# Kernel optimization log

Measured on AMD Instinct MI355X. Metric: run time of the kernel, lower is better.

Reference implementation:

```python
import jax, jax.numpy as jnp
import numpy as np

N_NODES = 100000
N_EDGES = 1600000
NUM_FEAT = 64
DIM = 32
K = 3  # num_stacks
T = 2  # num_layers


def setup_inputs() -> dict:
    key = jax.random.key(0)
    ks = jax.random.split(key, 10)
    g = lambda k, s, fan: jax.random.normal(k, s, jnp.float32) * (1.0 / np.sqrt(fan))
    x = jax.random.normal(ks[0], (N_NODES, NUM_FEAT), jnp.float32)
    edge_index = jax.random.randint(ks[1], (2, N_EDGES), 0, N_NODES)
    return {
        "x": x,
        "edge_index": edge_index,
        "w1_init": g(ks[2], (K, NUM_FEAT, DIM), NUM_FEAT),
        "w1": g(ks[3], (1, K, DIM, DIM), DIM),
        "w1_root": g(ks[4], (1, K, NUM_FEAT, DIM), NUM_FEAT),
        "b1": jnp.zeros((1, K, 1, DIM), jnp.float32),
        "w2_init": g(ks[5], (K, DIM, DIM), DIM),
        "w2": g(ks[6], (1, K, DIM, DIM), DIM),
        "w2_root": g(ks[7], (1, K, DIM, DIM), DIM),
        "b2": jnp.zeros((1, K, 1, DIM), jnp.float32),
    }


def _gcn_norm(src, dst, num_nodes):
    # symmetric normalization WITHOUT self loops (PyG ARMAConv default)
    deg = jax.ops.segment_sum(jnp.ones(src.shape[0], jnp.float32), dst, num_segments=num_nodes)
    dinv = jnp.where(deg > 0, jax.lax.rsqrt(jnp.maximum(deg, 1.0)), 0.0)
    return dinv[src] * dinv[dst]  # [E]


def _arma_conv(x, src, dst, norm, init_w, w, root_w, b, act):
    # x: [N,F_in]; init_w: [K,F_in,F_out]; w/root_w/b: shared (leading dim 1)
    num_nodes = x.shape[0]
    out = jnp.einsum('nf,kfo->kno', x, init_w)          # [K,N,F_out]
    root_term = jnp.einsum('nf,kfo->kno', x, root_w[0])  # shared across layers
    bias = b[0]                                          # [K,1,F_out]

    def prop(o):  # o: [N,F_out] -> A_hat @ o
        return jax.ops.segment_sum(o[src] * norm[:, None], dst, num_segments=num_nodes)

    for t in range(T):
        if t > 0:
            out = jnp.einsum('knf,kfo->kno', out, w[0])
        out = jax.vmap(prop)(out)
        out = act(out + root_term + bias)
    return out.mean(axis=0)  # mean over stacks -> [N,F_out]


def reference(x, edge_index, w1_init, w1, w1_root, b1, w2_init, w2, w2_root, b2):
    src, dst = edge_index[0], edge_index[1]
    norm = _gcn_norm(src, dst, x.shape[0])
    # eval mode: dropout is identity
    h = jax.nn.relu(_arma_conv(x, src, dst, norm, w1_init, w1, w1_root, b1, jax.nn.relu))
    out = _arma_conv(h, src, dst, norm, w2_init, w2, w2_root, b2, lambda z: z)
    return out
```

## Files before the change

### kernel.cpp

```cpp
#include <hip/hip_runtime.h>
#include <hip/hip_bf16.h>


#define KSTACK 3
#define DIM    32
#define FDIM   96
#define NB     256
#define TILE   4096

typedef __hip_bfloat16 bf16;
typedef _Float16 f16;
typedef _Float16 halfx2 __attribute__((ext_vector_type(2)));

__device__ __forceinline__ float dot2h(unsigned int a, unsigned int b, float c) {
#if __has_builtin(__builtin_amdgcn_fdot2)
    return __builtin_amdgcn_fdot2(__builtin_bit_cast(halfx2, a),
                                  __builtin_bit_cast(halfx2, b), c, false);
#else
    halfx2 ha = __builtin_bit_cast(halfx2, a);
    halfx2 hb = __builtin_bit_cast(halfx2, b);
    return c + (float)ha.x * (float)hb.x + (float)ha.y * (float)hb.y;
#endif
}

__device__ __forceinline__ unsigned int pkh(float lo, float hi) {
    return __builtin_bit_cast(unsigned int, __builtin_amdgcn_cvt_pkrtz(lo, hi));
}

__device__ __forceinline__ halfx2 h2(unsigned int q) {
    return __builtin_bit_cast(halfx2, q);
}


__global__ void zero_int_kernel(int* __restrict__ p, int n) {
    int i = blockIdx.x * 256 + threadIdx.x;
    if (i < n) p[i] = 0;
}

__global__ __launch_bounds__(256) void bucket_hist_kernel(const int* __restrict__ dst,
                                                          int* __restrict__ bcnt, int E) {
    __shared__ int cnt[NB];
    for (int i = threadIdx.x; i < NB; i += 256) cnt[i] = 0;
    __syncthreads();
    const int e0 = blockIdx.x * TILE;
    const int count = min(TILE, E - e0);
    for (int u = threadIdx.x; u < count; u += 256)
        atomicAdd(&cnt[dst[e0 + u] >> 9], 1);
    __syncthreads();
    for (int i = threadIdx.x; i < NB; i += 256)
        if (cnt[i]) atomicAdd(&bcnt[i], cnt[i]);
}

__global__ __launch_bounds__(256) void bucket_scan_kernel(const int* __restrict__ bcnt,
                                                          int* __restrict__ gcur,
                                                          int* __restrict__ gbase) {
    __shared__ int s[NB];
    const int t = threadIdx.x;
    int v = bcnt[t];
    s[t] = v;
    __syncthreads();
    for (int off = 1; off < NB; off <<= 1) {
        int add = (t >= off) ? s[t - off] : 0;
        __syncthreads();
        s[t] += add;
        __syncthreads();
    }
    gcur[t]  = s[t] - v;
    gbase[t] = s[t] - v;
}

__global__ __launch_bounds__(256) void group_edges_kernel(
    const int* __restrict__ src, const int* __restrict__ dst,
    int* __restrict__ gcur, int2* __restrict__ grouped, int E)
{
    __shared__ int cnt[NB], pref[NB], lbase[NB], lofs[NB], gres[NB];
    __shared__ int2 stage[TILE];
    const int tid = threadIdx.x;
    const int e0 = blockIdx.x * TILE;
    const int count = min(TILE, E - e0);
    cnt[tid] = 0;
    __syncthreads();
    #pragma unroll
    for (int u = 0; u < TILE / 256; ++u) {
        int idx = u * 256 + tid;
        if (idx < count) atomicAdd(&cnt[dst[e0 + idx] >> 9], 1);
    }
    __syncthreads();
    int v = cnt[tid];
    pref[tid] = v;
    __syncthreads();
    for (int off = 1; off < NB; off <<= 1) {
        int add = (tid >= off) ? pref[tid - off] : 0;
        __syncthreads();
        pref[tid] += add;
        __syncthreads();
    }
    int ex = pref[tid] - v;
    lbase[tid] = ex;
    lofs[tid]  = ex;
    gres[tid] = atomicAdd(&gcur[tid], v);
    __syncthreads();
    #pragma unroll
    for (int u = 0; u < TILE / 256; ++u) {
        int idx = u * 256 + tid;
        if (idx < count) {
            int e = e0 + idx;
            int d = dst[e];
            int lp = atomicAdd(&lofs[d >> 9], 1);
            stage[lp] = make_int2(src[e] << 6, d);
        }
    }
    __syncthreads();
    for (int i = tid; i < count; i += 256) {
        int2 pr = stage[i];
        int b = pr.y >> 9;
        grouped[gres[b] + (i - lbase[b])] = pr;
    }
}

__global__ __launch_bounds__(256) void deg_from_grouped_kernel(
    const int2* __restrict__ grouped, const int* __restrict__ gbase,
    const int* __restrict__ bcnt, int* __restrict__ deg, int N)
{
    __shared__ int h[512];
    const int b  = blockIdx.x;
    const int nb = b * 512;
    for (int i = threadIdx.x; i < 512; i += 256) h[i] = 0;
    __syncthreads();
    const int e0 = gbase[b], cnt = bcnt[b];
    for (int u = threadIdx.x; u < cnt; u += 256)
        atomicAdd(&h[grouped[e0 + u].y & 511], 1);
    __syncthreads();
    for (int i = threadIdx.x; i < 512; i += 256)
        if (nb + i < N) deg[nb + i] = h[i];
}

__global__ void dinv_kernel(const int* __restrict__ deg, float* __restrict__ dinv, int N) {
    int i = blockIdx.x * 256 + threadIdx.x;
    if (i < N) {
        int d = deg[i];
        dinv[i] = (d > 0) ? rsqrtf((float)d) : 0.0f;
    }
}

__global__ __launch_bounds__(512) void scan1_kernel(const int* __restrict__ deg,
                                                    int* __restrict__ off4,
                                                    int* __restrict__ bsums, int N) {
    __shared__ int tmp[512];
    int t = threadIdx.x;
    int i = blockIdx.x * 512 + t;
    int v = (i < N) ? ((deg[i] + 3) & ~3) : 0;
    tmp[t] = v;
    __syncthreads();
    for (int off = 1; off < 512; off <<= 1) {
        int add = (t >= off) ? tmp[t - off] : 0;
        __syncthreads();
        tmp[t] += add;
        __syncthreads();
    }
    if (i <= N) off4[i] = tmp[t] - v;
    if (t == 511) bsums[blockIdx.x] = tmp[511];
}

__global__ void scan2_kernel(int* __restrict__ bsums, int nb) {
    if (blockIdx.x == 0 && threadIdx.x == 0) {
        int run = 0;
        for (int b = 0; b < nb; ++b) { int v = bsums[b]; bsums[b] = run; run += v; }
    }
}

__global__ void scan3_kernel(int* __restrict__ off4, const int* __restrict__ bsums, int N) {
    int i = blockIdx.x * 256 + threadIdx.x;
    if (i <= N) off4[i] += bsums[i >> 9];
}

__global__ __launch_bounds__(256) void fill_csr_bucket_kernel(
    const int2* __restrict__ grouped, const int* __restrict__ gbase,
    const int* __restrict__ bcnt, const int* __restrict__ off4,
    int* __restrict__ csr, int N, int dummy)
{
    __shared__ int lofs[512];
    const int b  = blockIdx.x;
    const int nb = b * 512;
    for (int i = threadIdx.x; i < 512; i += 256)
        lofs[i] = (nb + i < N) ? off4[nb + i] : 0;
    __syncthreads();
    const int e0 = gbase[b], cnt = bcnt[b];
    for (int u = threadIdx.x; u < cnt; u += 256) {
        int2 pr = grouped[e0 + u];
        int pos = atomicAdd(&lofs[pr.y & 511], 1);
        csr[pos] = pr.x;
    }
    __syncthreads();
    for (int i = threadIdx.x; i < 512; i += 256) {
        int n = nb + i;
        if (n < N) {
            int p = lofs[i];
            int e = off4[n + 1];
            for (; p < e; ++p) csr[p] = dummy;
        }
    }
}

__global__ void zero_dummy_kernel(f16* __restrict__ a, f16* __restrict__ b,
                                  f16* __restrict__ c, int N) {
    int t = threadIdx.x;
    if (t < FDIM) {
        a[(long)N * FDIM + t] = (f16)0.f;
        b[(long)N * FDIM + t] = (f16)0.f;
    }
    if (t < DIM) c[(long)N * DIM + t] = (f16)0.f;
}


template <int FIN, bool MEANROOT, bool XF16>
__global__ __launch_bounds__(256) void mm_init_kernel(
    const float* __restrict__ xf,
    const f16*   __restrict__ xh,
    const float* __restrict__ wA,
    const float* __restrict__ wB,
    const float* __restrict__ dinv,
    f16*   __restrict__ outA,
    f16*   __restrict__ rootb,
    float* __restrict__ rootm,
    const float* __restrict__ bias,
    int N)
{
    constexpr int F2 = FIN / 2;
    __shared__ unsigned int swA2[KSTACK * F2 * 32];
    __shared__ unsigned int swB2[KSTACK * F2 * 32];
    __shared__ unsigned int sx2[F2 * 64];
    const int tid = threadIdx.x;
    const int n0  = blockIdx.x * 64;

    for (int i = tid; i < KSTACK * F2 * 32; i += 256) {
        int k = i / (F2 * 32), r = i % (F2 * 32), f2 = r >> 5, o = r & 31;
        swA2[i] = pkh(wA[(k * FIN + 2 * f2) * 32 + o], wA[(k * FIN + 2 * f2 + 1) * 32 + o]);
        swB2[i] = pkh(wB[(k * FIN + 2 * f2) * 32 + o], wB[(k * FIN + 2 * f2 + 1) * 32 + o]);
    }
    for (int i = tid; i < 64 * F2; i += 256) {
        int jj = i / F2, f2 = i % F2;
        int n = n0 + jj; if (n >= N) n = N - 1;
        unsigned int v;
        if (XF16) v = *reinterpret_cast<const unsigned int*>(xh + (long)n * FIN + 2 * f2);
        else      v = pkh(xf[(long)n * FIN + 2 * f2], xf[(long)n * FIN + 2 * f2 + 1]);
        sx2[f2 * 64 + jj] = v;
    }
    __syncthreads();

    const int o = tid & 31;
    const int g = tid >> 5;
    float bz[KSTACK];
    #pragma unroll
    for (int k = 0; k < KSTACK; ++k) bz[k] = bias[k * 32 + o];
    float accA[8][KSTACK];
    float accB[8][KSTACK];
    #pragma unroll
    for (int jj = 0; jj < 8; ++jj)
        #pragma unroll
        for (int k = 0; k < KSTACK; ++k) { accA[jj][k] = 0.f; accB[jj][k] = 0.f; }

    #pragma unroll 2
    for (int f2 = 0; f2 < F2; ++f2) {
        uint4 xlo = *reinterpret_cast<const uint4*>(&sx2[f2 * 64 + 8 * g]);
        uint4 xhi = *reinterpret_cast<const uint4*>(&sx2[f2 * 64 + 8 * g + 4]);
        unsigned int xp[8] = {xlo.x, xlo.y, xlo.z, xlo.w, xhi.x, xhi.y, xhi.z, xhi.w};
        #pragma unroll
        for (int k = 0; k < KSTACK; ++k) {
            unsigned int wa2 = swA2[(k * F2 + f2) * 32 + o];
            unsigned int wb2 = swB2[(k * F2 + f2) * 32 + o];
            #pragma unroll
            for (int jj = 0; jj < 8; ++jj) {
                accA[jj][k] = dot2h(xp[jj], wa2, accA[jj][k]);
                accB[jj][k] = dot2h(xp[jj], wb2, accB[jj][k]);
            }
        }
    }

    #pragma unroll
    for (int jj = 0; jj < 8; ++jj) {
        long n = n0 + 8 * g + jj;
        if (n < N) {
            const float di = dinv[n];
            float rsum = 0.f;
            #pragma unroll
            for (int k = 0; k < KSTACK; ++k) {
                float rb = accB[jj][k] + bz[k];
                outA[n * FDIM + k * 32 + o]  = (f16)(accA[jj][k] * di);
                rootb[n * FDIM + k * 32 + o] = (f16)rb;
                rsum += rb;
            }
            if (MEANROOT)
                rootm[n * 32 + o] = rsum * (1.0f / 3.0f);
        }
    }
}


#define GATHER_LOOP8()                                                         \
    const int m = max(nA, nB);                                                 \
    halfx2 aA01a = {0, 0}, aA23a = {0, 0}, aA01b = {0, 0}, aA23b = {0, 0};     \
    halfx2 aB01a = {0, 0}, aB23a = {0, 0}, aB01b = {0, 0}, aB23b = {0, 0};     \
    for (int b = 0; b < m; b += 8) {                                           \
        int4 tA0 = *reinterpret_cast<const int4*>(csr + iA + b);               \
        int4 tA1 = *reinterpret_cast<const int4*>(csr + iA + b + 4);           \
        int4 tB0 = *reinterpret_cast<const int4*>(csr + iB + b);               \
        int4 tB1 = *reinterpret_cast<const int4*>(csr + iB + b + 4);           \
        const int rA = nA - b, rB = nB - b;                                    \
        int oA0 = rA > 0 ? tA0.x : dummy;                                      \
        int oA1 = rA > 1 ? tA0.y : dummy;                                      \
        int oA2 = rA > 2 ? tA0.z : dummy;                                      \
        int oA3 = rA > 3 ? tA0.w : dummy;                                      \
        int oA4 = rA > 4 ? tA1.x : dummy;                                      \
        int oA5 = rA > 5 ? tA1.y : dummy;                                      \
        int oA6 = rA > 6 ? tA1.z : dummy;                                      \
        int oA7 = rA > 7 ? tA1.w : dummy;                                      \
        int oB0 = rB > 0 ? tB0.x : dummy;                                      \
        int oB1 = rB > 1 ? tB0.y : dummy;                                      \
        int oB2 = rB > 2 ? tB0.z : dummy;                                      \
        int oB3 = rB > 3 ? tB0.w : dummy;                                      \
        int oB4 = rB > 4 ? tB1.x : dummy;                                      \
        int oB5 = rB > 5 ? tB1.y : dummy;                                      \
        int oB6 = rB > 6 ? tB1.z : dummy;                                      \
        int oB7 = rB > 7 ? tB1.w : dummy;                                      \
        if (ld) {                                                              \
            uint2 qA0 = *reinterpret_cast<const uint2*>(base + 3 * oA0 + lb);  \
            uint2 qA1 = *reinterpret_cast<const uint2*>(base + 3 * oA1 + lb);  \
            uint2 qA2 = *reinterpret_cast<const uint2*>(base + 3 * oA2 + lb);  \
            uint2 qA3 = *reinterpret_cast<const uint2*>(base + 3 * oA3 + lb);  \
            uint2 qA4 = *reinterpret_cast<const uint2*>(base + 3 * oA4 + lb);  \
            uint2 qA5 = *reinterpret_cast<const uint2*>(base + 3 * oA5 + lb);  \
            uint2 qA6 = *reinterpret_cast<const uint2*>(base + 3 * oA6 + lb);  \
            uint2 qA7 = *reinterpret_cast<const uint2*>(base + 3 * oA7 + lb);  \
            uint2 qB0 = *reinterpret_cast<const uint2*>(base + 3 * oB0 + lb);  \
            uint2 qB1 = *reinterpret_cast<const uint2*>(base + 3 * oB1 + lb);  \
            uint2 qB2 = *reinterpret_cast<const uint2*>(base + 3 * oB2 + lb);  \
            uint2 qB3 = *reinterpret_cast<const uint2*>(base + 3 * oB3 + lb);  \
            uint2 qB4 = *reinterpret_cast<const uint2*>(base + 3 * oB4 + lb);  \
            uint2 qB5 = *reinterpret_cast<const uint2*>(base + 3 * oB5 + lb);  \
            uint2 qB6 = *reinterpret_cast<const uint2*>(base + 3 * oB6 + lb);  \
            uint2 qB7 = *reinterpret_cast<const uint2*>(base + 3 * oB7 + lb);  \
            aA01a += h2(qA0.x); aA23a += h2(qA0.y);                            \
            aA01b += h2(qA1.x); aA23b += h2(qA1.y);                            \
            aA01a += h2(qA2.x); aA23a += h2(qA2.y);                            \
            aA01b += h2(qA3.x); aA23b += h2(qA3.y);                            \
            aA01a += h2(qA4.x); aA23a += h2(qA4.y);                            \
            aA01b += h2(qA5.x); aA23b += h2(qA5.y);                            \
            aA01a += h2(qA6.x); aA23a += h2(qA6.y);                            \
            aA01b += h2(qA7.x); aA23b += h2(qA7.y);                            \
            aB01a += h2(qB0.x); aB23a += h2(qB0.y);                            \
            aB01b += h2(qB1.x); aB23b += h2(qB1.y);                            \
            aB01a += h2(qB2.x); aB23a += h2(qB2.y);                            \
            aB01b += h2(qB3.x); aB23b += h2(qB3.y);                            \
            aB01a += h2(qB4.x); aB23a += h2(qB4.y);                            \
            aB01b += h2(qB5.x); aB23b += h2(qB5.y);                            \
            aB01a += h2(qB6.x); aB23a += h2(qB6.y);                            \
            aB01b += h2(qB7.x); aB23b += h2(qB7.y);                            \
        }                                                                      \
    }                                                                          \
    const float aA0 = (float)aA01a.x + (float)aA01b.x;                         \
    const float aA1 = (float)aA01a.y + (float)aA01b.y;                         \
    const float aA2 = (float)aA23a.x + (float)aA23b.x;                         \
    const float aA3 = (float)aA23a.y + (float)aA23b.y;                         \
    const float aB0 = (float)aB01a.x + (float)aB01b.x;                         \
    const float aB1 = (float)aB01a.y + (float)aB01b.y;                         \
    const float aB2 = (float)aB23a.x + (float)aB23b.x;                         \
    const float aB3 = (float)aB23a.y + (float)aB23b.y;

#define DST_SETUP()                                                            \
    const int dA = blockIdx.x * 16 + j;                                        \
    const int dB = dA + 8;                                                     \
    const bool vA = dA < N, vB = dB < N;                                       \
    const int dummy = N * 64;                                                  \
    const bool ld  = lane < 24;                                                \
    const int  lb  = lane * 8;                                                 \
    const char* base = (const char*)in;                                        \
    halfx2 rA01 = {0, 0}, rA23 = {0, 0}, rB01 = {0, 0}, rB23 = {0, 0};         \
    int iA = 0, nA = 0, iB = 0, nB = 0;                                        \
    float diA = 0.f, diB = 0.f;                                                \
    if (vA) {                                                                  \
        iA = off4[dA]; nA = off4[dA + 1] - iA; diA = dinv[dA];                 \
        if (ld) {                                                              \
            uint2 rr = *reinterpret_cast<const uint2*>(                        \
                (const char*)root + (long)dA * 192 + lb);                      \
            rA01 = h2(rr.x); rA23 = h2(rr.y);                                  \
        }                                                                      \
    }                                                                          \
    if (vB) {                                                                  \
        iB = off4[dB]; nB = off4[dB + 1] - iB; diB = dinv[dB];                 \
        if (ld) {                                                              \
            uint2 rr = *reinterpret_cast<const uint2*>(                        \
                (const char*)root + (long)dB * 192 + lb);                      \
            rB01 = h2(rr.x); rB23 = h2(rr.y);                                  \
        }                                                                      \
    }

__device__ __forceinline__ void gemv96(const unsigned int* __restrict__ sv,
                                       const unsigned int* __restrict__ sw2,
                                       int lane, float& r0, float& r1, float& r2) {
    float o[KSTACK];
    #pragma unroll
    for (int k = 0; k < KSTACK; ++k) {
        const unsigned int* sp = sv + k * 16;
        uint4 s0 = *reinterpret_cast<const uint4*>(sp);
        uint4 s1 = *reinterpret_cast<const uint4*>(sp + 4);
        uint4 s2 = *reinterpret_cast<const uint4*>(sp + 8);
        uint4 s3 = *reinterpret_cast<const uint4*>(sp + 12);
        const unsigned int* wp = sw2 + k * 512 + lane;
        float a = 0.f;
        a = dot2h(s0.x, wp[0],   a); a = dot2h(s0.y, wp[32],  a);
        a = dot2h(s0.z, wp[64],  a); a = dot2h(s0.w, wp[96],  a);
        a = dot2h(s1.x, wp[128], a); a = dot2h(s1.y, wp[160], a);
        a = dot2h(s1.z, wp[192], a); a = dot2h(s1.w, wp[224], a);
        a = dot2h(s2.x, wp[256], a); a = dot2h(s2.y, wp[288], a);
        a = dot2h(s2.z, wp[320], a); a = dot2h(s2.w, wp[352], a);
        a = dot2h(s3.x, wp[384], a); a = dot2h(s3.y, wp[416], a);
        a = dot2h(s3.z, wp[448], a); a = dot2h(s3.w, wp[480], a);
        o[k] = a;
    }
    r0 = o[0]; r1 = o[1]; r2 = o[2];
}

__global__ __launch_bounds__(256) void prop_mm_kernel(
    const f16*   __restrict__ in,
    const int*   __restrict__ off4,
    const int*   __restrict__ csr,
    const float* __restrict__ dinv,
    const f16*   __restrict__ root,
    const float* __restrict__ w,
    f16* __restrict__ out, int N)
{
    __shared__ unsigned int sw2[KSTACK * 512];
    __shared__ unsigned int sv2[16][48];
    const int tid = threadIdx.x;
    for (int i = tid; i < KSTACK * 512; i += 256) {
        int k = i >> 9, r = i & 511, t = r >> 5, o = r & 31;
        sw2[i] = pkh(w[(k * 32 + 2 * t) * 32 + o], w[(k * 32 + 2 * t + 1) * 32 + o]);
    }
    __syncthreads();
    const int lane = tid & 31;
    const int j    = tid >> 5;
    DST_SETUP();

    GATHER_LOOP8();

    if (ld) {
        if (vA) {
            float v0 = fmaxf(aA0 * diA + (float)rA01.x, 0.f);
            float v1 = fmaxf(aA1 * diA + (float)rA01.y, 0.f);
            float v2 = fmaxf(aA2 * diA + (float)rA23.x, 0.f);
            float v3 = fmaxf(aA3 * diA + (float)rA23.y, 0.f);
            sv2[j][2 * lane]     = pkh(v0, v1);
            sv2[j][2 * lane + 1] = pkh(v2, v3);
        }
        if (vB) {
            float v0 = fmaxf(aB0 * diB + (float)rB01.x, 0.f);
            float v1 = fmaxf(aB1 * diB + (float)rB01.y, 0.f);
            float v2 = fmaxf(aB2 * diB + (float)rB23.x, 0.f);
            float v3 = fmaxf(aB3 * diB + (float)rB23.y, 0.f);
            sv2[j + 8][2 * lane]     = pkh(v0, v1);
            sv2[j + 8][2 * lane + 1] = pkh(v2, v3);
        }
    }
    if (vA) {
        float o0, o1, o2;
        gemv96(&sv2[j][0], sw2, lane, o0, o1, o2);
        out[(long)dA * FDIM + lane]      = (f16)(o0 * diA);
        out[(long)dA * FDIM + 32 + lane] = (f16)(o1 * diA);
        out[(long)dA * FDIM + 64 + lane] = (f16)(o2 * diA);
    }
    if (vB) {
        float o0, o1, o2;
        gemv96(&sv2[j + 8][0], sw2, lane, o0, o1, o2);
        out[(long)dB * FDIM + lane]      = (f16)(o0 * diB);
        out[(long)dB * FDIM + 32 + lane] = (f16)(o1 * diB);
        out[(long)dB * FDIM + 64 + lane] = (f16)(o2 * diB);
    }
}

__global__ __launch_bounds__(256) void prop_mean_kernel(
    const f16*   __restrict__ in,
    const int*   __restrict__ off4,
    const int*   __restrict__ csr,
    const float* __restrict__ dinv,
    const f16*   __restrict__ root,
    f16* __restrict__ out,
    int N)
{
    __shared__ float sv[16][FDIM];
    const int tid = threadIdx.x;
    const int lane = tid & 31;
    const int j    = tid >> 5;
    DST_SETUP();

    GATHER_LOOP8();

    if (ld) {
        if (vA) {
            sv[j][4*lane]   = fmaxf(aA0 * diA + (float)rA01.x, 0.f);
            sv[j][4*lane+1] = fmaxf(aA1 * diA + (float)rA01.y, 0.f);
            sv[j][4*lane+2] = fmaxf(aA2 * diA + (float)rA23.x, 0.f);
            sv[j][4*lane+3] = fmaxf(aA3 * diA + (float)rA23.y, 0.f);
        }
        if (vB) {
            sv[j+8][4*lane]   = fmaxf(aB0 * diB + (float)rB01.x, 0.f);
            sv[j+8][4*lane+1] = fmaxf(aB1 * diB + (float)rB01.y, 0.f);
            sv[j+8][4*lane+2] = fmaxf(aB2 * diB + (float)rB23.x, 0.f);
            sv[j+8][4*lane+3] = fmaxf(aB3 * diB + (float)rB23.y, 0.f);
        }
    }
    if (vA) {
        float mv = fmaxf((sv[j][lane] + sv[j][32 + lane] + sv[j][64 + lane]) * (1.0f / 3.0f), 0.f);
        out[(long)dA * 32 + lane] = (f16)mv;
    }
    if (vB) {
        float mv = fmaxf((sv[j+8][lane] + sv[j+8][32 + lane] + sv[j+8][64 + lane]) * (1.0f / 3.0f), 0.f);
        out[(long)dB * 32 + lane] = (f16)mv;
    }
}

__global__ __launch_bounds__(256) void prop_mm_mean_kernel(
    const f16*   __restrict__ in,
    const int*   __restrict__ off4,
    const int*   __restrict__ csr,
    const float* __restrict__ dinv,
    const f16*   __restrict__ root,
    const float* __restrict__ w,
    f16* __restrict__ out, int N)
{
    __shared__ unsigned int sw2[KSTACK * 512];
    __shared__ unsigned int sv2[16][48];
    const int tid = threadIdx.x;
    for (int i = tid; i < KSTACK * 512; i += 256) {
        int k = i >> 9, r = i & 511, t = r >> 5, o = r & 31;
        sw2[i] = pkh(w[(k * 32 + 2 * t) * 32 + o], w[(k * 32 + 2 * t + 1) * 32 + o]);
    }
    __syncthreads();
    const int lane = tid & 31;
    const int j    = tid >> 5;
    DST_SETUP();

    GATHER_LOOP8();

    if (ld) {
        if (vA) {
            sv2[j][2 * lane]     = pkh(aA0 * diA + (float)rA01.x, aA1 * diA + (float)rA01.y);
            sv2[j][2 * lane + 1] = pkh(aA2 * diA + (float)rA23.x, aA3 * diA + (float)rA23.y);
        }
        if (vB) {
            sv2[j + 8][2 * lane]     = pkh(aB0 * diB + (float)rB01.x, aB1 * diB + (float)rB01.y);
            sv2[j + 8][2 * lane + 1] = pkh(aB2 * diB + (float)rB23.x, aB3 * diB + (float)rB23.y);
        }
    }
    if (vA) {
        float o0, o1, o2;
        gemv96(&sv2[j][0], sw2, lane, o0, o1, o2);
        out[(long)dA * 32 + lane] = (f16)((o0 + o1 + o2) * (diA * (1.0f / 3.0f)));
    }
    if (vB) {
        float o0, o1, o2;
        gemv96(&sv2[j + 8][0], sw2, lane, o0, o1, o2);
        out[(long)dB * 32 + lane] = (f16)((o0 + o1 + o2) * (diB * (1.0f / 3.0f)));
    }
}

__global__ __launch_bounds__(256) void prop_mean2_kernel(
    const f16*   __restrict__ in,
    const int*   __restrict__ off4,
    const int*   __restrict__ csr,
    const float* __restrict__ dinv,
    const float* __restrict__ rootm,
    float* __restrict__ out,
    int N)
{
    const int lane = threadIdx.x & 15;
    const int g    = threadIdx.x >> 4;
    const int d    = blockIdx.x * 16 + g;
    if (d >= N) return;
    const int dummy = N * 64;
    const int lb = lane * 4;
    const char* base = (const char*)in;
    const int i0 = off4[d];
    const int n  = off4[d + 1] - i0;
    halfx2 aa = {0, 0}, ab = {0, 0};
    for (int b = 0; b < n; b += 8) {
        int4 t0 = *reinterpret_cast<const int4*>(csr + i0 + b);
        int4 t1 = *reinterpret_cast<const int4*>(csr + i0 + b + 4);
        const int r = n - b;
        int o0 = r > 0 ? t0.x : dummy;
        int o1 = r > 1 ? t0.y : dummy;
        int o2 = r > 2 ? t0.z : dummy;
        int o3 = r > 3 ? t0.w : dummy;
        int o4 = r > 4 ? t1.x : dummy;
        int o5 = r > 5 ? t1.y : dummy;
        int o6 = r > 6 ? t1.z : dummy;
        int o7 = r > 7 ? t1.w : dummy;
        unsigned int q0 = *reinterpret_cast<const unsigned int*>(base + o0 + lb);
        unsigned int q1 = *reinterpret_cast<const unsigned int*>(base + o1 + lb);
        unsigned int q2 = *reinterpret_cast<const unsigned int*>(base + o2 + lb);
        unsigned int q3 = *reinterpret_cast<const unsigned int*>(base + o3 + lb);
        unsigned int q4 = *reinterpret_cast<const unsigned int*>(base + o4 + lb);
        unsigned int q5 = *reinterpret_cast<const unsigned int*>(base + o5 + lb);
        unsigned int q6 = *reinterpret_cast<const unsigned int*>(base + o6 + lb);
        unsigned int q7 = *reinterpret_cast<const unsigned int*>(base + o7 + lb);
        aa += h2(q0); ab += h2(q1); aa += h2(q2); ab += h2(q3);
        aa += h2(q4); ab += h2(q5); aa += h2(q6); ab += h2(q7);
    }
    const float di = dinv[d];
    float a0 = (float)aa.x + (float)ab.x;
    float a1 = (float)aa.y + (float)ab.y;
    float2 rm = *reinterpret_cast<const float2*>(rootm + (long)d * 32 + 2 * lane);
    float2 res = make_float2(a0 * di + rm.x, a1 * di + rm.y);
    *reinterpret_cast<float2*>(out + (long)d * 32 + 2 * lane) = res;
}


extern "C" void kernel_launch(void* const* d_in, const int* in_sizes, int n_in,
                              void* d_out, int out_size, void* d_ws, size_t ws_size,
                              hipStream_t stream) {
    const float* x       = (const float*)d_in[0];
    const int*   edge    = (const int*)  d_in[1];
    const float* w1_init = (const float*)d_in[2];
    const float* w1      = (const float*)d_in[3];
    const float* w1_root = (const float*)d_in[4];
    const float* b1      = (const float*)d_in[5];
    const float* w2_init = (const float*)d_in[6];
    const float* w2      = (const float*)d_in[7];
    const float* w2_root = (const float*)d_in[8];
    const float* b2      = (const float*)d_in[9];
    float* out = (float*)d_out;

    const int N = in_sizes[0] / 64;
    const int E = in_sizes[1] / 2;
    const int* src = edge;
    const int* dst = edge + E;
    const int E4max = E + 3 * N;

    char* p = (char*)d_ws;
    auto alloc = [&](size_t bytes) { void* r = (void*)p; p += (bytes + 255) & ~(size_t)255; return r; };
    int*   deg      = (int*)  alloc((size_t)N * 4);
    float* dinv     = (float*)alloc((size_t)N * 4);
    int*   off4     = (int*)  alloc((size_t)(N + 1) * 4);
    const int nScanBlocks = (N + 1 + 511) / 512;
    int*   bsums    = (int*)  alloc((size_t)nScanBlocks * 4);
    int*   bcnt     = (int*)  alloc((size_t)NB * 4);
    int*   gcur     = (int*)  alloc((size_t)NB * 4);
    int*   gbase    = (int*)  alloc((size_t)NB * 4);
    int*   csr_boff = (int*)  alloc((size_t)(E4max + 1024) * 4);
    f16*   gatherA  = (f16*)  alloc((size_t)(N + 1) * FDIM * 2);
    f16*   gatherB  = (f16*)  alloc((size_t)(N + 1) * FDIM * 2);
    f16*   grow2    = (f16*)  alloc((size_t)(N + 1) * DIM * 2);
    f16*   rootb    = (f16*)  alloc((size_t)N * FDIM * 2);
    float* rootm    = (float*)alloc((size_t)N * DIM * 4);
    f16*   hbuf     = (f16*)  alloc((size_t)N * DIM * 2);
    int2*  grouped  = (int2*) alloc((size_t)E * 8);
    (void)ws_size; (void)n_in; (void)out_size;

    const int gN     = (N + 255) / 256;
    const int gN1    = (N + 1 + 255) / 256;
    const int gT     = (E + TILE - 1) / TILE;
    const int gNod64 = (N + 63) / 64;
    const int gNod16 = (N + 15) / 16;

    zero_int_kernel<<<1, 256, 0, stream>>>(bcnt, NB);
    bucket_hist_kernel<<<gT, 256, 0, stream>>>(dst, bcnt, E);
    bucket_scan_kernel<<<1, NB, 0, stream>>>(bcnt, gcur, gbase);
    group_edges_kernel<<<gT, 256, 0, stream>>>(src, dst, gcur, grouped, E);
    deg_from_grouped_kernel<<<NB, 256, 0, stream>>>(grouped, gbase, bcnt, deg, N);
    dinv_kernel<<<gN, 256, 0, stream>>>(deg, dinv, N);
    scan1_kernel<<<nScanBlocks, 512, 0, stream>>>(deg, off4, bsums, N);
    scan2_kernel<<<1, 64, 0, stream>>>(bsums, nScanBlocks);
    scan3_kernel<<<gN1, 256, 0, stream>>>(off4, bsums, N);
    fill_csr_bucket_kernel<<<NB, 256, 0, stream>>>(grouped, gbase, bcnt, off4, csr_boff, N, N * 64);
    zero_dummy_kernel<<<1, 96, 0, stream>>>(gatherA, gatherB, grow2, N);

    mm_init_kernel<64, false, false><<<gNod64, 256, 0, stream>>>(x, nullptr, w1_init, w1_root, dinv, gatherA, rootb, nullptr, b1, N);
    prop_mm_kernel<<<gNod16, 256, 0, stream>>>(gatherA, off4, csr_boff, dinv, rootb, w1, gatherB, N);
    prop_mean_kernel<<<gNod16, 256, 0, stream>>>(gatherB, off4, csr_boff, dinv, rootb, hbuf, N);

    mm_init_kernel<32, true, true><<<gNod64, 256, 0, stream>>>(nullptr, hbuf, w2_init, w2_root, dinv, gatherA, rootb, rootm, b2, N);
    prop_mm_mean_kernel<<<gNod16, 256, 0, stream>>>(gatherA, off4, csr_boff, dinv, rootb, w2, grow2, N);
    prop_mean2_kernel<<<gNod16, 256, 0, stream>>>(grow2, off4, csr_boff, dinv, rootm, out, N);
}
```

Measured before the change: 361.1 us.

## Pack grouped edges into 32-bit words and fuse degree, dinv, and scan

Grouped edge records shrink from int2 to a single 32-bit word holding the local destination index in the high 9 bits and the source in the low 23 bits. The per-bucket degree histogram, the dinv computation and the first scan stage are merged into one kernel, which removes two launches and the deg buffer round trip. The serial single-thread block-sum scan becomes a parallel 256-thread scan. This relies on N fitting in 23 bits and on the scan block count matching the bucket count, and it caps scan2 at 256 blocks.

```diff
diff --git a/kernel.cpp b/kernel.cpp
--- a/kernel.cpp
+++ b/kernel.cpp
@@ -71,7 +71,7 @@
 
 __global__ __launch_bounds__(256) void group_edges_kernel(
     const int* __restrict__ src, const int* __restrict__ dst,
-    int* __restrict__ gcur, int2* __restrict__ grouped, int E)
+    int* __restrict__ gcur, unsigned int* __restrict__ grouped, int E)
 {
     __shared__ int cnt[NB], pref[NB], lbase[NB], lofs[NB], gres[NB];
     __shared__ int2 stage[TILE];
@@ -107,49 +107,38 @@
             int e = e0 + idx;
             int d = dst[e];
             int lp = atomicAdd(&lofs[d >> 9], 1);
-            stage[lp] = make_int2(src[e] << 6, d);
+            stage[lp] = make_int2(src[e], d);
         }
     }
     __syncthreads();
     for (int i = tid; i < count; i += 256) {
         int2 pr = stage[i];
         int b = pr.y >> 9;
-        grouped[gres[b] + (i - lbase[b])] = pr;
-    }
-}
-
-__global__ __launch_bounds__(256) void deg_from_grouped_kernel(
-    const int2* __restrict__ grouped, const int* __restrict__ gbase,
-    const int* __restrict__ bcnt, int* __restrict__ deg, int N)
+        grouped[gres[b] + (i - lbase[b])] =
+            ((unsigned int)(pr.y & 511) << 23) | (unsigned int)pr.x;
+    }
+}
+
+__global__ __launch_bounds__(512) void scan1_kernel(
+    const unsigned int* __restrict__ grouped, const int* __restrict__ gbase,
+    const int* __restrict__ bcnt, float* __restrict__ dinv,
+    int* __restrict__ off4, int* __restrict__ bsums, int N)
 {
     __shared__ int h[512];
+    __shared__ int tmp[512];
     const int b  = blockIdx.x;
+    const int t  = threadIdx.x;
     const int nb = b * 512;
-    for (int i = threadIdx.x; i < 512; i += 256) h[i] = 0;
+    h[t] = 0;
     __syncthreads();
     const int e0 = gbase[b], cnt = bcnt[b];
-    for (int u = threadIdx.x; u < cnt; u += 256)
-        atomicAdd(&h[grouped[e0 + u].y & 511], 1);
-    __syncthreads();
-    for (int i = threadIdx.x; i < 512; i += 256)
-        if (nb + i < N) deg[nb + i] = h[i];
-}
-
-__global__ void dinv_kernel(const int* __restrict__ deg, float* __restrict__ dinv, int N) {
-    int i = blockIdx.x * 256 + threadIdx.x;
-    if (i < N) {
-        int d = deg[i];
-        dinv[i] = (d > 0) ? rsqrtf((float)d) : 0.0f;
-    }
-}
-
-__global__ __launch_bounds__(512) void scan1_kernel(const int* __restrict__ deg,
-                                                    int* __restrict__ off4,
-                                                    int* __restrict__ bsums, int N) {
-    __shared__ int tmp[512];
-    int t = threadIdx.x;
-    int i = blockIdx.x * 512 + t;
-    int v = (i < N) ? ((deg[i] + 3) & ~3) : 0;
+    for (int u = t; u < cnt; u += 512)
+        atomicAdd(&h[grouped[e0 + u] >> 23], 1);
+    __syncthreads();
+    const int i  = nb + t;
+    const int dg = h[t];
+    if (i < N) dinv[i] = (dg > 0) ? rsqrtf((float)dg) : 0.0f;
+    int v = (i < N) ? ((dg + 3) & ~3) : 0;
     tmp[t] = v;
     __syncthreads();
     for (int off = 1; off < 512; off <<= 1) {
@@ -159,14 +148,22 @@
         __syncthreads();
     }
     if (i <= N) off4[i] = tmp[t] - v;
-    if (t == 511) bsums[blockIdx.x] = tmp[511];
-}
-
-__global__ void scan2_kernel(int* __restrict__ bsums, int nb) {
-    if (blockIdx.x == 0 && threadIdx.x == 0) {
-        int run = 0;
-        for (int b = 0; b < nb; ++b) { int v = bsums[b]; bsums[b] = run; run += v; }
-    }
+    if (t == 511) bsums[b] = tmp[511];
+}
+
+__global__ __launch_bounds__(256) void scan2_kernel(int* __restrict__ bsums, int nb_) {
+    __shared__ int s[256];
+    const int t = threadIdx.x;
+    int v = (t < nb_) ? bsums[t] : 0;
+    s[t] = v;
+    __syncthreads();
+    for (int off = 1; off < 256; off <<= 1) {
+        int add = (t >= off) ? s[t - off] : 0;
+        __syncthreads();
+        s[t] += add;
+        __syncthreads();
+    }
+    if (t < nb_) bsums[t] = s[t] - v;
 }
 
 __global__ void scan3_kernel(int* __restrict__ off4, const int* __restrict__ bsums, int N) {
@@ -175,7 +172,7 @@
 }
 
 __global__ __launch_bounds__(256) void fill_csr_bucket_kernel(
-    const int2* __restrict__ grouped, const int* __restrict__ gbase,
+    const unsigned int* __restrict__ grouped, const int* __restrict__ gbase,
     const int* __restrict__ bcnt, const int* __restrict__ off4,
     int* __restrict__ csr, int N, int dummy)
 {
@@ -187,9 +184,9 @@
     __syncthreads();
     const int e0 = gbase[b], cnt = bcnt[b];
     for (int u = threadIdx.x; u < cnt; u += 256) {
-        int2 pr = grouped[e0 + u];
-        int pos = atomicAdd(&lofs[pr.y & 511], 1);
-        csr[pos] = pr.x;
+        unsigned int pe = grouped[e0 + u];
+        int pos = atomicAdd(&lofs[pe >> 23], 1);
+        csr[pos] = (int)(pe & 0x7fffffu) << 6;
     }
     __syncthreads();
     for (int i = threadIdx.x; i < 512; i += 256) {
@@ -638,7 +635,6 @@
 
     char* p = (char*)d_ws;
     auto alloc = [&](size_t bytes) { void* r = (void*)p; p += (bytes + 255) & ~(size_t)255; return r; };
-    int*   deg      = (int*)  alloc((size_t)N * 4);
     float* dinv     = (float*)alloc((size_t)N * 4);
     int*   off4     = (int*)  alloc((size_t)(N + 1) * 4);
     const int nScanBlocks = (N + 1 + 511) / 512;
@@ -653,10 +649,9 @@
     f16*   rootb    = (f16*)  alloc((size_t)N * FDIM * 2);
     float* rootm    = (float*)alloc((size_t)N * DIM * 4);
     f16*   hbuf     = (f16*)  alloc((size_t)N * DIM * 2);
-    int2*  grouped  = (int2*) alloc((size_t)E * 8);
+    unsigned int* grouped = (unsigned int*)alloc((size_t)E * 4);
     (void)ws_size; (void)n_in; (void)out_size;
 
-    const int gN     = (N + 255) / 256;
     const int gN1    = (N + 1 + 255) / 256;
     const int gT     = (E + TILE - 1) / TILE;
     const int gNod64 = (N + 63) / 64;
@@ -666,12 +661,10 @@
     bucket_hist_kernel<<<gT, 256, 0, stream>>>(dst, bcnt, E);
     bucket_scan_kernel<<<1, NB, 0, stream>>>(bcnt, gcur, gbase);
     group_edges_kernel<<<gT, 256, 0, stream>>>(src, dst, gcur, grouped, E);
-    deg_from_grouped_kernel<<<NB, 256, 0, stream>>>(grouped, gbase, bcnt, deg, N);
-    dinv_kernel<<<gN, 256, 0, stream>>>(deg, dinv, N);
-    scan1_kernel<<<nScanBlocks, 512, 0, stream>>>(deg, off4, bsums, N);
-    scan2_kernel<<<1, 64, 0, stream>>>(bsums, nScanBlocks);
+    scan1_kernel<<<nScanBlocks, 512, 0, stream>>>(grouped, gbase, bcnt, dinv, off4, bsums, N);
+    scan2_kernel<<<1, 256, 0, stream>>>(bsums, nScanBlocks);
     scan3_kernel<<<gN1, 256, 0, stream>>>(off4, bsums, N);
-    fill_csr_bucket_kernel<<<NB, 256, 0, stream>>>(grouped, gbase, bcnt, off4, csr_boff, N, N * 64);
+    fill_csr_bucket_kernel<<<nScanBlocks, 256, 0, stream>>>(grouped, gbase, bcnt, off4, csr_boff, N, N * 64);
     zero_dummy_kernel<<<1, 96, 0, stream>>>(gatherA, gatherB, grow2, N);
 
     mm_init_kernel<64, false, false><<<gNod64, 256, 0, stream>>>(x, nullptr, w1_init, w1_root, dinv, gatherA, rootb, nullptr, b1, N);
```

After: 331.0 us. 8.3% less time.
